# Optimization experiments

Measured on AMD Instinct MI355X. Metric: run time of the kernel, lower is better.

The kernel has to match this reference:

```python
import jax, jax.numpy as jnp
import numpy as np

D_MODEL = 512
NUM_HEADS = 8


def setup_inputs() -> dict:
    key = jax.random.key(0)
    ks = jax.random.split(key, 12)
    B, S, D = 2, 4096, D_MODEL
    scale = 1.0 / np.sqrt(D)
    inp = {
        "q": jax.random.normal(ks[0], (B, S, D), jnp.float32),
        "k": jax.random.normal(ks[1], (B, S, D), jnp.float32),
        "v": jax.random.normal(ks[2], (B, S, D), jnp.float32),
        "w_q": jax.random.normal(ks[3], (D, D), jnp.float32) * scale,
        "b_q": jax.random.normal(ks[4], (D,), jnp.float32) * scale,
        "w_k": jax.random.normal(ks[5], (D, D), jnp.float32) * scale,
        "b_k": jax.random.normal(ks[6], (D,), jnp.float32) * scale,
        "w_v": jax.random.normal(ks[7], (D, D), jnp.float32) * scale,
        "b_v": jax.random.normal(ks[8], (D,), jnp.float32) * scale,
        "w_o": jax.random.normal(ks[9], (D, D), jnp.float32) * scale,
        "b_o": jax.random.normal(ks[10], (D,), jnp.float32) * scale,
    }
    return inp


def _split_heads(x, h):
    b, s, d = x.shape
    return x.reshape(b, s, h, d // h).transpose(0, 2, 1, 3)  # [B,H,S,dk]


def reference(q, k, v, w_q, b_q, w_k, b_k, w_v, b_v, w_o, b_o):
    h = NUM_HEADS
    # Linear projections (torch Linear: x @ W.T + b)
    qh = _split_heads(q @ w_q.T + b_q, h)
    kh = _split_heads(k @ w_k.T + b_k, h)
    vh = _split_heads(v @ w_v.T + b_v, h)
    d_k = kh.shape[-1]
    scores = jnp.einsum("bhsd,bhtd->bhst", qh, kh) / jnp.sqrt(jnp.float32(d_k))
    attn = jax.nn.softmax(scores, axis=-1)  # [B,H,S,S] - materialized, as in source
    out = jnp.einsum("bhst,bhtd->bhsd", attn, vh)
    b, _, s, dk = out.shape
    out = out.transpose(0, 2, 1, 3).reshape(b, s, h * dk)
    return out @ w_o.T + b_o
```

## Files before the change

### kernel.cpp

```cpp
#include <hip/hip_runtime.h>
#include <hip/hip_bf16.h>

#define D_MODEL 512
#define NHEAD   8
#define DK      64
#define SEQ     4096
#define BATCH   2
#define NTOK    (BATCH * SEQ)

typedef __bf16 bf16;
typedef __bf16 bf16x4 __attribute__((ext_vector_type(4)));
typedef __bf16 bf16x8 __attribute__((ext_vector_type(8)));
typedef float  f32x4  __attribute__((ext_vector_type(4)));
typedef float  f32x16 __attribute__((ext_vector_type(16)));

#define MFMA16(a, b, c) __builtin_amdgcn_mfma_f32_16x16x32_bf16((a), (b), (c), 0, 0, 0)
#define MFMA32(a, b, c) __builtin_amdgcn_mfma_f32_32x32x16_bf16((a), (b), (c), 0, 0, 0)

#define QSCALE 0.18033688f

__global__ __launch_bounds__(256) void cvt_w(
    const float* __restrict__ wq, const float* __restrict__ wk,
    const float* __restrict__ wv, const float* __restrict__ wo,
    bf16* __restrict__ Wb)
{
    int i = blockIdx.x * 256 + threadIdx.x;
    int m = i >> 16;
    int g = i & 65535;
    const float* src = (m == 0) ? wq : (m == 1) ? wk : (m == 2) ? wv : wo;
    float4 x = *(const float4*)(src + (size_t)g * 4);
    bf16x4 y = {(bf16)x.x, (bf16)x.y, (bf16)x.z, (bf16)x.w};
    *(bf16x4*)(Wb + (size_t)m * D_MODEL * D_MODEL + (size_t)g * 4) = y;
}

__global__ __launch_bounds__(256, 3) void proj_qkv(
    const float* __restrict__ q, const float* __restrict__ k, const float* __restrict__ v,
    const bf16* __restrict__ Wb,
    const float* __restrict__ bq, const float* __restrict__ bk, const float* __restrict__ bv,
    bf16* __restrict__ Qh, bf16* __restrict__ Kh, bf16* __restrict__ Vt)
{
    const int p = blockIdx.z;
    const float* X    = (p == 0) ? q  : (p == 1) ? k  : v;
    const bf16*  W    = Wb + (size_t)p * D_MODEL * D_MODEL;
    const float* bias = (p == 0) ? bq : (p == 1) ? bk : bv;

    __shared__ union __align__(16) {
        struct { bf16 As[128][72]; bf16 Bs[128][72]; } g;
        bf16 T[128][136];
    } sm;

    const int m0   = blockIdx.x * 128;
    const int n0   = blockIdx.y * 128;
    const int tid  = threadIdx.x;
    const int lane = tid & 63;
    const int wave = tid >> 6;
    const int low4 = lane & 15;
    const int quad = lane >> 4;
    const int wm   = wave >> 1;
    const int wn   = wave & 1;

    int srow[8], sc4[8];
    for (int it = 0; it < 8; ++it) {
        int idx = tid + it * 256;
        srow[it] = idx >> 4;
        sc4[it]  = (idx & 15) * 4;
    }
    int br[4], bc[4];
    for (int it = 0; it < 4; ++it) {
        int idx = tid + it * 256;
        br[it] = idx >> 3;
        bc[it] = (idx & 7) * 8;
    }

    float4 gA[8];
    bf16x8 gB[4];
    for (int it = 0; it < 8; ++it)
        gA[it] = *(const float4*)(X + (size_t)(m0 + srow[it]) * D_MODEL + sc4[it]);
    for (int it = 0; it < 4; ++it)
        gB[it] = *(const bf16x8*)(W + (size_t)(n0 + br[it]) * D_MODEL + bc[it]);

    f32x4 acc[4][4];
    for (int i = 0; i < 4; ++i)
        for (int j = 0; j < 4; ++j)
            acc[i][j] = f32x4{0.f, 0.f, 0.f, 0.f};

    for (int k0 = 0; k0 < D_MODEL; k0 += 64) {
        __syncthreads();
        for (int it = 0; it < 8; ++it) {
            bf16x4 wa = {(bf16)gA[it].x, (bf16)gA[it].y, (bf16)gA[it].z, (bf16)gA[it].w};
            *(bf16x4*)&sm.g.As[srow[it]][sc4[it]] = wa;
        }
        for (int it = 0; it < 4; ++it)
            *(bf16x8*)&sm.g.Bs[br[it]][bc[it]] = gB[it];
        __syncthreads();

        if (k0 + 64 < D_MODEL) {
            for (int it = 0; it < 8; ++it)
                gA[it] = *(const float4*)(X + (size_t)(m0 + srow[it]) * D_MODEL + k0 + 64 + sc4[it]);
            for (int it = 0; it < 4; ++it)
                gB[it] = *(const bf16x8*)(W + (size_t)(n0 + br[it]) * D_MODEL + k0 + 64 + bc[it]);
        }

        for (int ks = 0; ks < 2; ++ks) {
            bf16x8 a[4], b[4];
            for (int i = 0; i < 4; ++i)
                a[i] = *(const bf16x8*)&sm.g.As[wm * 64 + i * 16 + low4][ks * 32 + quad * 8];
            for (int j = 0; j < 4; ++j)
                b[j] = *(const bf16x8*)&sm.g.Bs[wn * 64 + j * 16 + low4][ks * 32 + quad * 8];
            for (int i = 0; i < 4; ++i)
                for (int j = 0; j < 4; ++j)
                    acc[i][j] = MFMA16(a[i], b[j], acc[i][j]);
        }
    }

    if (p < 2) {
        bf16* Out = (p == 0) ? Qh : Kh;
        const float sc = (p == 0) ? QSCALE : 1.0f;
        for (int j = 0; j < 4; ++j) {
            int col = n0 + wn * 64 + j * 16 + low4;
            float bcol = bias[col];
            for (int i = 0; i < 4; ++i)
                for (int r = 0; r < 4; ++r) {
                    int row = m0 + wm * 64 + i * 16 + quad * 4 + r;
                    Out[(size_t)row * D_MODEL + col] = (bf16)((acc[i][j][r] + bcol) * sc);
                }
        }
    } else {
        __syncthreads();
        for (int j = 0; j < 4; ++j) {
            int col = n0 + wn * 64 + j * 16 + low4;
            float bcol = bias[col];
            for (int i = 0; i < 4; ++i)
                for (int r = 0; r < 4; ++r)
                    sm.T[wn * 64 + j * 16 + low4][wm * 64 + i * 16 + quad * 4 + r] =
                        (bf16)(acc[i][j][r] + bcol);
        }
        __syncthreads();
        const int bb = m0 >> 12;
        const int s0 = (m0 & 4095);
        for (int it = 0; it < 8; ++it) {
            int cc = it * 16 + (tid >> 4);
            int ml = (tid & 15) * 8;
            int col = n0 + cc;
            int hh = col >> 6, dd = col & 63;
            *(bf16x8*)&Vt[(((size_t)(bb * NHEAD + hh) * DK + dd) << 12) + s0 + ml] =
                *(const bf16x8*)&sm.T[cc][ml];
        }
    }
}

__global__ __launch_bounds__(512, 4) void attn(
    const bf16* __restrict__ Qh, const bf16* __restrict__ Kh,
    const bf16* __restrict__ Vt, bf16* __restrict__ O)
{
    __shared__ union __align__(16) {
        struct { bf16 Ks[128][72]; bf16 Vs[64][136]; } s;
        float Obuf[4][32][68];
    } sm;
    __shared__ bf16  Ps[8][32][72];
    __shared__ float Lbuf[4][32];

    const int q0   = blockIdx.x * 128;
    const int bh   = blockIdx.y;
    const int b    = bh >> 3, h = bh & 7;
    const int tid  = threadIdx.x;
    const int lane = tid & 63;
    const int wave = tid >> 6;
    const int qg   = wave >> 1;
    const int kg   = wave & 1;
    const int m32  = lane & 31;
    const int hl   = lane >> 5;

    const bf16* Kbase = Kh + (size_t)b * SEQ * D_MODEL + h * DK;
    const bf16* Vbase = Vt + (size_t)bh * DK * SEQ;

    const bf16* Qrow = Qh + (size_t)(b * SEQ + q0 + qg * 32 + m32) * D_MODEL + h * DK;
    bf16x8 qf[4];
    for (int ks = 0; ks < 4; ++ks)
        qf[ks] = *(const bf16x8*)(Qrow + ks * 16 + hl * 8);

    float l = 0.f;
    f32x16 acc[2];
    for (int i = 0; i < 16; ++i) { acc[0][i] = 0.f; acc[1][i] = 0.f; }

    int kr[2], kc[2], vr[2], vc[2];
    for (int it = 0; it < 2; ++it) {
        int c = tid + it * 512;
        kr[it] = c >> 3;  kc[it] = (c & 7) * 8;
        vr[it] = c >> 4;  vc[it] = (c & 15) * 8;
    }
    bf16x8 gk[2], gv[2];
    for (int it = 0; it < 2; ++it) {
        gk[it] = *(const bf16x8*)(Kbase + (size_t)kr[it] * D_MODEL + kc[it]);
        gv[it] = *(const bf16x8*)(Vbase + (size_t)vr[it] * SEQ + vc[it]);
    }

    for (int t0 = 0; t0 < SEQ; t0 += 128) {
        __syncthreads();
        for (int it = 0; it < 2; ++it) {
            *(bf16x8*)&sm.s.Ks[kr[it]][kc[it]] = gk[it];
            *(bf16x8*)&sm.s.Vs[vr[it]][vc[it]] = gv[it];
        }
        __syncthreads();

        if (t0 + 128 < SEQ) {
            for (int it = 0; it < 2; ++it) {
                gk[it] = *(const bf16x8*)(Kbase + (size_t)(t0 + 128 + kr[it]) * D_MODEL + kc[it]);
                gv[it] = *(const bf16x8*)(Vbase + (size_t)vr[it] * SEQ + t0 + 128 + vc[it]);
            }
        }

        for (int mt = 0; mt < 2; ++mt) {
            f32x16 sc;
            for (int i = 0; i < 16; ++i) sc[i] = 0.f;
            for (int ks = 0; ks < 4; ++ks) {
                bf16x8 kf = *(const bf16x8*)&sm.s.Ks[kg * 64 + mt * 32 + m32][ks * 16 + hl * 8];
                sc = MFMA32(kf, qf[ks], sc);
            }
            for (int g = 0; g < 4; ++g) {
                float p0 = __builtin_amdgcn_exp2f(sc[g * 4 + 0]);
                float p1 = __builtin_amdgcn_exp2f(sc[g * 4 + 1]);
                float p2 = __builtin_amdgcn_exp2f(sc[g * 4 + 2]);
                float p3 = __builtin_amdgcn_exp2f(sc[g * 4 + 3]);
                l += (p0 + p1) + (p2 + p3);
                bf16x4 pw = {(bf16)p0, (bf16)p1, (bf16)p2, (bf16)p3};
                *(bf16x4*)&Ps[wave][m32][mt * 32 + g * 8 + hl * 4] = pw;
            }
        }

        for (int ks = 0; ks < 4; ++ks) {
            bf16x8 pf = *(const bf16x8*)&Ps[wave][m32][ks * 16 + hl * 8];
            for (int nt = 0; nt < 2; ++nt) {
                bf16x8 vfr = *(const bf16x8*)&sm.s.Vs[nt * 32 + m32][kg * 64 + ks * 16 + hl * 8];
                acc[nt] = MFMA32(pf, vfr, acc[nt]);
            }
        }
    }

    l += __shfl_xor(l, 32);
    __syncthreads();
    if (kg == 1) {
        for (int nt = 0; nt < 2; ++nt)
            for (int r = 0; r < 16; ++r) {
                int qq = (r & 3) + 8 * (r >> 2) + 4 * hl;
                sm.Obuf[qg][qq][nt * 32 + m32] = acc[nt][r];
            }
        if (hl == 0) Lbuf[qg][m32] = l;
    }
    __syncthreads();
    if (kg == 0) {
        float lt  = l + Lbuf[qg][m32];
        float inv = 1.0f / lt;
        for (int nt = 0; nt < 2; ++nt)
            for (int r = 0; r < 16; ++r) {
                int qq = (r & 3) + 8 * (r >> 2) + 4 * hl;
                float val = acc[nt][r] + sm.Obuf[qg][qq][nt * 32 + m32];
                float iv  = __shfl(inv, qq);
                O[(size_t)(b * SEQ + q0 + qg * 32 + qq) * D_MODEL + h * DK + nt * 32 + m32] =
                    (bf16)(val * iv);
            }
    }
}

__global__ __launch_bounds__(256, 4) void proj_out(
    const bf16* __restrict__ Oin, const bf16* __restrict__ Wo,
    const float* __restrict__ bo, float* __restrict__ out)
{
    __shared__ bf16 As[64][72];
    __shared__ bf16 Bs[64][72];

    const int m0   = blockIdx.x * 64;
    const int n0   = blockIdx.y * 64;
    const int tid  = threadIdx.x;
    const int lane = tid & 63;
    const int wave = tid >> 6;
    const int low4 = lane & 15;
    const int quad = lane >> 4;
    const int wm   = wave >> 1;
    const int wn   = wave & 1;

    int arow[2], ag[2];
    for (int it = 0; it < 2; ++it) {
        int idx = tid + it * 256;
        arow[it] = idx >> 3;
        ag[it]   = (idx & 7) * 8;
    }

    bf16x8 gA[2], gB[2];
    for (int it = 0; it < 2; ++it) {
        gA[it] = *(const bf16x8*)(Oin + (size_t)(m0 + arow[it]) * D_MODEL + ag[it]);
        gB[it] = *(const bf16x8*)(Wo + (size_t)(n0 + arow[it]) * D_MODEL + ag[it]);
    }

    f32x4 acc[2][2];
    for (int i = 0; i < 2; ++i)
        for (int j = 0; j < 2; ++j)
            acc[i][j] = f32x4{0.f, 0.f, 0.f, 0.f};

    for (int k0 = 0; k0 < D_MODEL; k0 += 64) {
        __syncthreads();
        for (int it = 0; it < 2; ++it) {
            *(bf16x8*)&As[arow[it]][ag[it]] = gA[it];
            *(bf16x8*)&Bs[arow[it]][ag[it]] = gB[it];
        }
        __syncthreads();

        if (k0 + 64 < D_MODEL) {
            for (int it = 0; it < 2; ++it) {
                gA[it] = *(const bf16x8*)(Oin + (size_t)(m0 + arow[it]) * D_MODEL + k0 + 64 + ag[it]);
                gB[it] = *(const bf16x8*)(Wo + (size_t)(n0 + arow[it]) * D_MODEL + k0 + 64 + ag[it]);
            }
        }

        for (int ks = 0; ks < 2; ++ks) {
            bf16x8 a[2], b[2];
            for (int i = 0; i < 2; ++i)
                a[i] = *(const bf16x8*)&As[wm * 32 + i * 16 + low4][ks * 32 + quad * 8];
            for (int j = 0; j < 2; ++j)
                b[j] = *(const bf16x8*)&Bs[wn * 32 + j * 16 + low4][ks * 32 + quad * 8];
            for (int i = 0; i < 2; ++i)
                for (int j = 0; j < 2; ++j)
                    acc[i][j] = MFMA16(a[i], b[j], acc[i][j]);
        }
    }

    for (int j = 0; j < 2; ++j) {
        int col = n0 + wn * 32 + j * 16 + low4;
        float bcol = bo[col];
        for (int i = 0; i < 2; ++i)
            for (int r = 0; r < 4; ++r) {
                int row = m0 + wm * 32 + i * 16 + quad * 4 + r;
                out[(size_t)row * D_MODEL + col] = acc[i][j][r] + bcol;
            }
    }
}

extern "C" void kernel_launch(void* const* d_in, const int* in_sizes, int n_in,
                              void* d_out, int out_size, void* d_ws, size_t ws_size,
                              hipStream_t stream)
{
    const float* q  = (const float*)d_in[0];
    const float* k  = (const float*)d_in[1];
    const float* v  = (const float*)d_in[2];
    const float* wq = (const float*)d_in[3];
    const float* bq = (const float*)d_in[4];
    const float* wk = (const float*)d_in[5];
    const float* bk = (const float*)d_in[6];
    const float* wv = (const float*)d_in[7];
    const float* bv = (const float*)d_in[8];
    const float* wo = (const float*)d_in[9];
    const float* bo = (const float*)d_in[10];

    const size_t NT = (size_t)NTOK * D_MODEL;
    bf16* Qh = (bf16*)d_ws;
    bf16* Kh = Qh + NT;
    bf16* Vt = Kh + NT;
    bf16* O  = Vt + NT;
    bf16* Wb = O + NT;

    cvt_w<<<1024, 256, 0, stream>>>(wq, wk, wv, wo, Wb);

    dim3 g1(NTOK / 128, D_MODEL / 128, 3);
    proj_qkv<<<g1, 256, 0, stream>>>(q, k, v, Wb, bq, bk, bv, Qh, Kh, Vt);

    dim3 g2(SEQ / 128, BATCH * NHEAD);
    attn<<<g2, 512, 0, stream>>>(Qh, Kh, Vt, O);

    dim3 g3(NTOK / 64, D_MODEL / 64);
    proj_out<<<g3, 256, 0, stream>>>(O, Wb + (size_t)3 * D_MODEL * D_MODEL, bo, (float*)d_out);
}
```

Measured before the change: 231.8 us.

## Give each attention wave two query tiles and remap block indices by head

The attention kernel drops from 512 to 256 threads per block. Each wave now handles two 32-row query tiles, so every K and V fragment read from shared memory is reused across both tiles and shared-memory traffic per MFMA goes down. The 1D grid is remapped so that a fixed (flat & 7) group of blocks covers two batch-heads, which appears aimed at the chiplet/L2 placement of K/V reuse. The cost is more registers per thread (more accumulators and cached fragments), lower occupancy via launch_bounds(256,2), and fewer waves to hide load and exp latency.

```diff
diff --git a/kernel.cpp b/kernel.cpp
--- a/kernel.cpp
+++ b/kernel.cpp
@@ -149,24 +149,26 @@
     }
 }
 
-__global__ __launch_bounds__(512, 4) void attn(
+__global__ __launch_bounds__(256, 2) void attn(
     const bf16* __restrict__ Qh, const bf16* __restrict__ Kh,
     const bf16* __restrict__ Vt, bf16* __restrict__ O)
 {
     __shared__ union __align__(16) {
         struct { bf16 Ks[128][72]; bf16 Vs[64][136]; } s;
-        float Obuf[4][32][68];
+        float Obuf[128][68];
     } sm;
-    __shared__ bf16  Ps[8][32][72];
-    __shared__ float Lbuf[4][32];
-
-    const int q0   = blockIdx.x * 128;
-    const int bh   = blockIdx.y;
+    __shared__ bf16  Ps[4][2][32][72];
+    __shared__ float Lbuf[2][2][32];
+
+    const int flat = blockIdx.x;
+    const int slot = flat >> 3;
+    const int bh   = (flat & 7) * 2 + (slot >> 5);
+    const int q0   = (slot & 31) * 128;
     const int b    = bh >> 3, h = bh & 7;
     const int tid  = threadIdx.x;
     const int lane = tid & 63;
     const int wave = tid >> 6;
-    const int qg   = wave >> 1;
+    const int qp   = wave >> 1;
     const int kg   = wave & 1;
     const int m32  = lane & 31;
     const int hl   = lane >> 5;
@@ -174,91 +176,110 @@
     const bf16* Kbase = Kh + (size_t)b * SEQ * D_MODEL + h * DK;
     const bf16* Vbase = Vt + (size_t)bh * DK * SEQ;
 
-    const bf16* Qrow = Qh + (size_t)(b * SEQ + q0 + qg * 32 + m32) * D_MODEL + h * DK;
-    bf16x8 qf[4];
-    for (int ks = 0; ks < 4; ++ks)
-        qf[ks] = *(const bf16x8*)(Qrow + ks * 16 + hl * 8);
-
-    float l = 0.f;
-    f32x16 acc[2];
-    for (int i = 0; i < 16; ++i) { acc[0][i] = 0.f; acc[1][i] = 0.f; }
-
-    int kr[2], kc[2], vr[2], vc[2];
-    for (int it = 0; it < 2; ++it) {
-        int c = tid + it * 512;
-        kr[it] = c >> 3;  kc[it] = (c & 7) * 8;
-        vr[it] = c >> 4;  vc[it] = (c & 15) * 8;
-    }
-    bf16x8 gk[2], gv[2];
-    for (int it = 0; it < 2; ++it) {
-        gk[it] = *(const bf16x8*)(Kbase + (size_t)kr[it] * D_MODEL + kc[it]);
-        gv[it] = *(const bf16x8*)(Vbase + (size_t)vr[it] * SEQ + vc[it]);
+    bf16x8 qf[2][4];
+    for (int qt = 0; qt < 2; ++qt) {
+        const bf16* Qrow = Qh + (size_t)(b * SEQ + q0 + qp * 64 + qt * 32 + m32) * D_MODEL + h * DK;
+        for (int ks = 0; ks < 4; ++ks)
+            qf[qt][ks] = *(const bf16x8*)(Qrow + ks * 16 + hl * 8);
+    }
+
+    float l[2] = {0.f, 0.f};
+    f32x16 acc[2][2];
+    for (int qt = 0; qt < 2; ++qt)
+        for (int nt = 0; nt < 2; ++nt)
+            for (int i = 0; i < 16; ++i) acc[qt][nt][i] = 0.f;
+
+    int krr[4], kcc[4], vrr[4], vcc[4];
+    for (int it = 0; it < 4; ++it) {
+        int idx = tid + it * 256;
+        krr[it] = idx >> 3;  kcc[it] = (idx & 7) * 8;
+        vrr[it] = idx >> 4;  vcc[it] = (idx & 15) * 8;
+    }
+    bf16x8 gk[4], gv[4];
+    for (int it = 0; it < 4; ++it) {
+        gk[it] = *(const bf16x8*)(Kbase + (size_t)krr[it] * D_MODEL + kcc[it]);
+        gv[it] = *(const bf16x8*)(Vbase + (size_t)vrr[it] * SEQ + vcc[it]);
     }
 
     for (int t0 = 0; t0 < SEQ; t0 += 128) {
         __syncthreads();
-        for (int it = 0; it < 2; ++it) {
-            *(bf16x8*)&sm.s.Ks[kr[it]][kc[it]] = gk[it];
-            *(bf16x8*)&sm.s.Vs[vr[it]][vc[it]] = gv[it];
+        for (int it = 0; it < 4; ++it) {
+            *(bf16x8*)&sm.s.Ks[krr[it]][kcc[it]] = gk[it];
+            *(bf16x8*)&sm.s.Vs[vrr[it]][vcc[it]] = gv[it];
         }
         __syncthreads();
 
         if (t0 + 128 < SEQ) {
-            for (int it = 0; it < 2; ++it) {
-                gk[it] = *(const bf16x8*)(Kbase + (size_t)(t0 + 128 + kr[it]) * D_MODEL + kc[it]);
-                gv[it] = *(const bf16x8*)(Vbase + (size_t)vr[it] * SEQ + t0 + 128 + vc[it]);
-            }
-        }
-
-        for (int mt = 0; mt < 2; ++mt) {
-            f32x16 sc;
-            for (int i = 0; i < 16; ++i) sc[i] = 0.f;
+            for (int it = 0; it < 4; ++it) {
+                gk[it] = *(const bf16x8*)(Kbase + (size_t)(t0 + 128 + krr[it]) * D_MODEL + kcc[it]);
+                gv[it] = *(const bf16x8*)(Vbase + (size_t)vrr[it] * SEQ + t0 + 128 + vcc[it]);
+            }
+        }
+
+        bf16x8 kf[2][4];
+        for (int mt = 0; mt < 2; ++mt)
+            for (int ks = 0; ks < 4; ++ks)
+                kf[mt][ks] = *(const bf16x8*)&sm.s.Ks[kg * 64 + mt * 32 + m32][ks * 16 + hl * 8];
+
+        for (int qt = 0; qt < 2; ++qt) {
+            f32x16 sc[2];
+            for (int mt = 0; mt < 2; ++mt) {
+                for (int i = 0; i < 16; ++i) sc[mt][i] = 0.f;
+                for (int ks = 0; ks < 4; ++ks)
+                    sc[mt] = MFMA32(kf[mt][ks], qf[qt][ks], sc[mt]);
+            }
+            for (int mt = 0; mt < 2; ++mt)
+                for (int g = 0; g < 4; ++g) {
+                    float p0 = __builtin_amdgcn_exp2f(sc[mt][g * 4 + 0]);
+                    float p1 = __builtin_amdgcn_exp2f(sc[mt][g * 4 + 1]);
+                    float p2 = __builtin_amdgcn_exp2f(sc[mt][g * 4 + 2]);
+                    float p3 = __builtin_amdgcn_exp2f(sc[mt][g * 4 + 3]);
+                    l[qt] += (p0 + p1) + (p2 + p3);
+                    bf16x4 pw = {(bf16)p0, (bf16)p1, (bf16)p2, (bf16)p3};
+                    *(bf16x4*)&Ps[wave][qt][m32][mt * 32 + g * 8 + hl * 4] = pw;
+                }
+        }
+
+        bf16x8 vf[2][4];
+        for (int nt = 0; nt < 2; ++nt)
+            for (int ks = 0; ks < 4; ++ks)
+                vf[nt][ks] = *(const bf16x8*)&sm.s.Vs[nt * 32 + m32][kg * 64 + ks * 16 + hl * 8];
+
+        for (int qt = 0; qt < 2; ++qt)
             for (int ks = 0; ks < 4; ++ks) {
-                bf16x8 kf = *(const bf16x8*)&sm.s.Ks[kg * 64 + mt * 32 + m32][ks * 16 + hl * 8];
-                sc = MFMA32(kf, qf[ks], sc);
-            }
-            for (int g = 0; g < 4; ++g) {
-                float p0 = __builtin_amdgcn_exp2f(sc[g * 4 + 0]);
-                float p1 = __builtin_amdgcn_exp2f(sc[g * 4 + 1]);
-                float p2 = __builtin_amdgcn_exp2f(sc[g * 4 + 2]);
-                float p3 = __builtin_amdgcn_exp2f(sc[g * 4 + 3]);
-                l += (p0 + p1) + (p2 + p3);
-                bf16x4 pw = {(bf16)p0, (bf16)p1, (bf16)p2, (bf16)p3};
-                *(bf16x4*)&Ps[wave][m32][mt * 32 + g * 8 + hl * 4] = pw;
-            }
-        }
-
-        for (int ks = 0; ks < 4; ++ks) {
-            bf16x8 pf = *(const bf16x8*)&Ps[wave][m32][ks * 16 + hl * 8];
-            for (int nt = 0; nt < 2; ++nt) {
-                bf16x8 vfr = *(const bf16x8*)&sm.s.Vs[nt * 32 + m32][kg * 64 + ks * 16 + hl * 8];
-                acc[nt] = MFMA32(pf, vfr, acc[nt]);
-            }
-        }
-    }
-
-    l += __shfl_xor(l, 32);
+                bf16x8 pf = *(const bf16x8*)&Ps[wave][qt][m32][ks * 16 + hl * 8];
+                for (int nt = 0; nt < 2; ++nt)
+                    acc[qt][nt] = MFMA32(pf, vf[nt][ks], acc[qt][nt]);
+            }
+    }
+
+    for (int qt = 0; qt < 2; ++qt)
+        l[qt] += __shfl_xor(l[qt], 32);
     __syncthreads();
     if (kg == 1) {
-        for (int nt = 0; nt < 2; ++nt)
-            for (int r = 0; r < 16; ++r) {
-                int qq = (r & 3) + 8 * (r >> 2) + 4 * hl;
-                sm.Obuf[qg][qq][nt * 32 + m32] = acc[nt][r];
-            }
-        if (hl == 0) Lbuf[qg][m32] = l;
+        for (int qt = 0; qt < 2; ++qt) {
+            for (int nt = 0; nt < 2; ++nt)
+                for (int r = 0; r < 16; ++r) {
+                    int qq = (r & 3) + 8 * (r >> 2) + 4 * hl;
+                    sm.Obuf[qp * 64 + qt * 32 + qq][nt * 32 + m32] = acc[qt][nt][r];
+                }
+            if (hl == 0) Lbuf[qp][qt][m32] = l[qt];
+        }
     }
     __syncthreads();
     if (kg == 0) {
-        float lt  = l + Lbuf[qg][m32];
-        float inv = 1.0f / lt;
-        for (int nt = 0; nt < 2; ++nt)
-            for (int r = 0; r < 16; ++r) {
-                int qq = (r & 3) + 8 * (r >> 2) + 4 * hl;
-                float val = acc[nt][r] + sm.Obuf[qg][qq][nt * 32 + m32];
-                float iv  = __shfl(inv, qq);
-                O[(size_t)(b * SEQ + q0 + qg * 32 + qq) * D_MODEL + h * DK + nt * 32 + m32] =
-                    (bf16)(val * iv);
-            }
+        for (int qt = 0; qt < 2; ++qt) {
+            float lt  = l[qt] + Lbuf[qp][qt][m32];
+            float inv = 1.0f / lt;
+            for (int nt = 0; nt < 2; ++nt)
+                for (int r = 0; r < 16; ++r) {
+                    int qq = (r & 3) + 8 * (r >> 2) + 4 * hl;
+                    float val = acc[qt][nt][r] + sm.Obuf[qp * 64 + qt * 32 + qq][nt * 32 + m32];
+                    float iv  = __shfl(inv, qq);
+                    O[(size_t)(b * SEQ + q0 + qp * 64 + qt * 32 + qq) * D_MODEL + h * DK + nt * 32 + m32] =
+                        (bf16)(val * iv);
+                }
+        }
     }
 }
 
@@ -363,8 +384,7 @@
     dim3 g1(NTOK / 128, D_MODEL / 128, 3);
     proj_qkv<<<g1, 256, 0, stream>>>(q, k, v, Wb, bq, bk, bv, Qh, Kh, Vt);
 
-    dim3 g2(SEQ / 128, BATCH * NHEAD);
-    attn<<<g2, 512, 0, stream>>>(Qh, Kh, Vt, O);
+    attn<<<512, 256, 0, stream>>>(Qh, Kh, Vt, O);
 
     dim3 g3(NTOK / 64, D_MODEL / 64);
     proj_out<<<g3, 256, 0, stream>>>(O, Wb + (size_t)3 * D_MODEL * D_MODEL, bo, (float*)d_out);
```

Measured after the change: 355.5 us. +53.4%, slower.
